# Kernel optimization log

Measured on AMD Instinct MI355X. Metric: run time of the kernel, lower is better.

The kernel has to match this reference:

```python
import jax, jax.numpy as jnp
import numpy as np

TAU = 0.5
EPS = 1e-12  # F.normalize eps


def _l2_normalize(z):
    n = jnp.linalg.norm(z, axis=1, keepdims=True)
    return z / jnp.maximum(n, EPS)


def _semi_loss(a, b):
    # a, b: [N, d], already raw embeddings; normalize then exp(sim/tau)
    an = _l2_normalize(a)
    bn = _l2_normalize(b)
    refl = jnp.exp(jnp.matmul(an, an.T) / TAU)      # [N, N]
    between = jnp.exp(jnp.matmul(an, bn.T) / TAU)   # [N, N]
    pos = jnp.diagonal(between)
    denom = refl.sum(axis=1) + between.sum(axis=1) - jnp.diagonal(refl)
    return -jnp.log(pos / denom)


def setup_inputs() -> dict:
    key = jax.random.key(0)
    k1, k2 = jax.random.split(key)
    z1 = jax.random.normal(k1, (8192, 256), dtype=jnp.float32)
    z2 = jax.random.normal(k2, (8192, 256), dtype=jnp.float32)
    return {"z1": z1, "z2": z2, "mean": 1}


def reference(z1, z2, mean):
    l1 = _semi_loss(z1, z2)
    l2 = _semi_loss(z2, z1)
    ret = (l1 + l2) * 0.5
    return ret.mean() if mean else ret.sum()
```

## Files before the change

kernel.cpp:

```cpp
#include <hip/hip_runtime.h>
#include <hip/hip_bf16.h>
#include <hip/hip_fp8.h>

#define N_ROWS 8192
#define NZ 16384
#define DIM 256
#define TAU_INV 2.0f
#define BT 128
#define NTILE 128
#define NTRI (NTILE * (NTILE + 1) / 2)
#define NCHUNK 16

typedef float f32x4 __attribute__((ext_vector_type(4)));
typedef long lx2 __attribute__((ext_vector_type(2)));

__global__ __launch_bounds__(256) void normalize_kernel(
    const float* __restrict__ z1, const float* __restrict__ z2,
    unsigned char* __restrict__ Z8, float* __restrict__ pos)
{
    const int tid = threadIdx.x;
    const int wave = tid >> 6;
    const int lane = tid & 63;
    const int row = blockIdx.x * 4 + wave;

    const float4 a = ((const float4*)(z1 + (size_t)row * DIM))[lane];
    const float4 b = ((const float4*)(z2 + (size_t)row * DIM))[lane];

    auto wsum = [&](float v) -> float {
        #pragma unroll
        for (int m = 1; m < 64; m <<= 1) v += __shfl_xor(v, m, 64);
        return v;
    };

    const float na2 = wsum(a.x*a.x + a.y*a.y + a.z*a.z + a.w*a.w);
    const float nb2 = wsum(b.x*b.x + b.y*b.y + b.z*b.z + b.w*b.w);
    const float sa = 16.0f / sqrtf(na2);
    const float sb = 16.0f / sqrtf(nb2);

    const float av[4] = {a.x*sa, a.y*sa, a.z*sa, a.w*sa};
    const float bv[4] = {b.x*sb, b.y*sb, b.z*sb, b.w*sb};
    unsigned char pa[4], pb[4];
    float qd = 0.0f;
    #pragma unroll
    for (int k = 0; k < 4; ++k) {
        __hip_fp8_e4m3 qa(av[k]);
        __hip_fp8_e4m3 qb(bv[k]);
        pa[k] = qa.__x; pb[k] = qb.__x;
        qd += float(qa) * float(qb);
    }
    const int g  = (lane >> 1) & 7;
    const int pp = ((g & 3) << 1) | (g >> 2);
    const int off = (lane >> 4) * 64 + pp * 8 + (lane & 1) * 4;
    *(uchar4*)(Z8 + (size_t)row * DIM + off) = *(uchar4*)pa;
    *(uchar4*)(Z8 + (size_t)(N_ROWS + row) * DIM + off) = *(uchar4*)pb;

    qd = wsum(qd);
    if (lane == 0) pos[row] = qd * 0.00390625f;
}

template <bool TWO_STAGE>
__global__ __launch_bounds__(256, 4) void gram_kernel(
    const unsigned char* __restrict__ Z,
    float* __restrict__ part, float* __restrict__ S)
{
    const int bid = (blockIdx.x & 7) * (NTRI / 8) + (blockIdx.x >> 3);
    int ti = (int)((257.0f - sqrtf(66049.0f - 8.0f * (float)bid)) * 0.5f);
    ti = ti < 0 ? 0 : (ti > 127 ? 127 : ti);
    while (ti * (257 - ti) / 2 > bid) --ti;
    while ((ti + 1) * (256 - ti) / 2 <= bid) ++ti;
    const int tj = ti + (bid - ti * (257 - ti) / 2);
    const bool diag = (ti == tj);

    __shared__ unsigned char Ls[32768];

    const int tid  = threadIdx.x;
    const int wave = tid >> 6;
    const int lane = tid & 63;
    const int wr = wave >> 1, wc = wave & 1;
    const int lm = lane & 15, lq = lane >> 4;

    const int r8 = lane >> 3;
    const int pg = lane & 7;
    const int G0 = pg ^ (r8 >> 1);
    const int dlt = 64 - ((G0 & 4) << 5);
    const unsigned char* pAE =
        Z + (size_t)(ti * BT + wave * 32 + r8) * DIM + (G0 << 4);
    const unsigned char* pBE =
        Z + (size_t)(tj * BT + wave * 32 + r8) * DIM + (G0 << 4);
    const unsigned char* pAO = pAE + dlt;
    const unsigned char* pBO = pBE + dlt;

    const int s0 = (lq ^ (lm >> 1)) << 4;
    const int s1 = s0 ^ 64;
    const unsigned char* LA0 = Ls + wr * 8192 + lm * 128 + s0;
    const unsigned char* LA1 = Ls + wr * 8192 + lm * 128 + s1;
    const unsigned char* LB0 = Ls + 16384 + wc * 8192 + lm * 128 + s0;
    const unsigned char* LB1 = Ls + 16384 + wc * 8192 + lm * 128 + s1;

    f32x4 acc[4][4] = {};

    #pragma unroll
    for (int kh = 0; kh < 2; ++kh) {
        if (kh) __syncthreads();
        #pragma unroll
        for (int c = 0; c < 4; ++c) {
            const int ld = (wave * 4 + c) * 1024;
            const unsigned char* ga = ((c & 1) ? pAO : pAE) + c * 2048 + kh * 128;
            const unsigned char* gb = ((c & 1) ? pBO : pBE) + c * 2048 + kh * 128;
            __builtin_amdgcn_global_load_lds(
                (const __attribute__((address_space(1))) void*)ga,
                (__attribute__((address_space(3))) void*)(Ls + ld), 16, 0, 0);
            __builtin_amdgcn_global_load_lds(
                (const __attribute__((address_space(1))) void*)gb,
                (__attribute__((address_space(3))) void*)(Ls + 16384 + ld), 16, 0, 0);
        }
        __syncthreads();

        lx2 aP[4], bP[4];
        #pragma unroll
        for (int f = 0; f < 4; ++f) {
            aP[f] = *(const lx2*)(LA0 + f * 2048);
            bP[f] = *(const lx2*)(LB0 + f * 2048);
        }
        #pragma unroll
        for (int fr = 0; fr < 4; ++fr)
            #pragma unroll
            for (int fc = 0; fc < 4; ++fc) {
                acc[fr][fc] = __builtin_amdgcn_mfma_f32_16x16x32_fp8_fp8(
                    aP[fr].x, bP[fc].x, acc[fr][fc], 0, 0, 0);
                acc[fr][fc] = __builtin_amdgcn_mfma_f32_16x16x32_fp8_fp8(
                    aP[fr].y, bP[fc].y, acc[fr][fc], 0, 0, 0);
            }
        #pragma unroll
        for (int f = 0; f < 4; ++f) {
            aP[f] = *(const lx2*)(LA1 + f * 2048);
            bP[f] = *(const lx2*)(LB1 + f * 2048);
        }
        #pragma unroll
        for (int fr = 0; fr < 4; ++fr)
            #pragma unroll
            for (int fc = 0; fc < 4; ++fc) {
                acc[fr][fc] = __builtin_amdgcn_mfma_f32_16x16x32_fp8_fp8(
                    aP[fr].x, bP[fc].x, acc[fr][fc], 0, 0, 0);
                acc[fr][fc] = __builtin_amdgcn_mfma_f32_16x16x32_fp8_fp8(
                    aP[fr].y, bP[fc].y, acc[fr][fc], 0, 0, 0);
            }
    }

    const float SC = 2.8853900817779268f / 256.0f;
    #pragma unroll
    for (int fr = 0; fr < 4; ++fr)
        #pragma unroll
        for (int fc = 0; fc < 4; ++fc)
            #pragma unroll
            for (int r = 0; r < 4; ++r)
                acc[fr][fc][r] = exp2f(acc[fr][fc][r] * SC);

    if (diag) {
        #pragma unroll
        for (int fr = 0; fr < 4; ++fr) {
            const int gi = wr * 64 + fr * 16 + lq * 4;
            #pragma unroll
            for (int fc = 0; fc < 4; ++fc) {
                const int gj = wc * 64 + fc * 16 + lm;
                #pragma unroll
                for (int r = 0; r < 4; ++r)
                    if (gj <= gi + r) acc[fr][fc][r] = 0.0f;
            }
        }
    }

    float* dst = TWO_STAGE ? (part + (size_t)bid * 512) : nullptr;

    #pragma unroll
    for (int fr = 0; fr < 4; ++fr)
        #pragma unroll
        for (int r = 0; r < 4; ++r) {
            float s = acc[fr][0][r] + acc[fr][1][r] + acc[fr][2][r] + acc[fr][3][r];
            s += __shfl_xor(s, 1, 64);
            s += __shfl_xor(s, 2, 64);
            s += __shfl_xor(s, 4, 64);
            s += __shfl_xor(s, 8, 64);
            if (lm == 0) {
                const int rr = wr * 64 + fr * 16 + lq * 4 + r;
                if (TWO_STAGE) dst[wc * 128 + rr] = s;
                else atomicAdd(&S[ti * BT + rr], s);
            }
        }
    #pragma unroll
    for (int fc = 0; fc < 4; ++fc) {
        float s = 0.0f;
        #pragma unroll
        for (int fr = 0; fr < 4; ++fr)
            #pragma unroll
            for (int r = 0; r < 4; ++r) s += acc[fr][fc][r];
        s += __shfl_xor(s, 16, 64);
        s += __shfl_xor(s, 32, 64);
        if (lq == 0) {
            const int cc = wc * 64 + fc * 16 + lm;
            if (TWO_STAGE) dst[256 + wr * 128 + cc] = s;
            else atomicAdd(&S[tj * BT + cc], s);
        }
    }
}

__global__ __launch_bounds__(256) void reduce_kernel(
    const float* __restrict__ part, float* __restrict__ S2,
    float* __restrict__ out)
{
    const int chunk = blockIdx.y;
    const int tid = threadIdx.x;
    const int r = blockIdx.x * 256 + tid;
    const int tr = r >> 7, rr = r & 127;
    const int baseRow = tr * (257 - tr) / 2;
    const int cntRow = 2 * (128 - tr);

    if (chunk == 0 && r == 0) out[0] = 0.0f;

    float s = 0.0f;
    for (int m = chunk; m < 258; m += NCHUNK) {
        size_t addr;
        if (m < cntRow) {
            const int bb = baseRow + (m >> 1);
            addr = (size_t)bb * 512 + (m & 1) * 128 + rr;
        } else {
            const int m2 = m - cntRow;
            const int tiq = m2 >> 1;
            const int bb = tiq * (257 - tiq) / 2 + (tr - tiq);
            addr = (size_t)bb * 512 + 256 + (m2 & 1) * 128 + rr;
        }
        s += part[addr];
    }
    S2[(size_t)chunk * NZ + r] = s;
}

__global__ __launch_bounds__(256) void loss2_kernel(
    const float* __restrict__ S2, const float* __restrict__ pos,
    float* __restrict__ out)
{
    const int i = blockIdx.x * 256 + threadIdx.x;
    float den1 = 0.0f, den2 = 0.0f;
    #pragma unroll
    for (int c = 0; c < NCHUNK; ++c) {
        den1 += S2[(size_t)c * NZ + i];
        den2 += S2[(size_t)c * NZ + N_ROWS + i];
    }
    float v = 0.5f * (logf(den1) + logf(den2)) - TAU_INV * pos[i];

    __shared__ float red[4];
    #pragma unroll
    for (int m = 1; m < 64; m <<= 1) v += __shfl_xor(v, m, 64);
    if ((threadIdx.x & 63) == 0) red[threadIdx.x >> 6] = v;
    __syncthreads();
    if (threadIdx.x == 0)
        atomicAdd(out, (red[0] + red[1] + red[2] + red[3]) * (1.0f / N_ROWS));
}

__global__ __launch_bounds__(256) void loss_kernel(
    const float* __restrict__ S, const float* __restrict__ pos,
    float* __restrict__ out)
{
    const int i = blockIdx.x * 256 + threadIdx.x;
    float v = 0.5f * (logf(S[i]) + logf(S[N_ROWS + i])) - TAU_INV * pos[i];

    __shared__ float red[4];
    #pragma unroll
    for (int m = 1; m < 64; m <<= 1) v += __shfl_xor(v, m, 64);
    if ((threadIdx.x & 63) == 0) red[threadIdx.x >> 6] = v;
    __syncthreads();
    if (threadIdx.x == 0)
        atomicAdd(out, (red[0] + red[1] + red[2] + red[3]) * (1.0f / N_ROWS));
}

extern "C" void kernel_launch(void* const* d_in, const int* in_sizes, int n_in,
                              void* d_out, int out_size, void* d_ws, size_t ws_size,
                              hipStream_t stream)
{
    const float* z1 = (const float*)d_in[0];
    const float* z2 = (const float*)d_in[1];
    float* out = (float*)d_out;

    char* ws = (char*)d_ws;
    unsigned char* Z8 = (unsigned char*)ws;
    float* pos  = (float*)(ws + 4194304);
    float* S2   = (float*)(ws + 4227072);
    float* part = (float*)(ws + 5275648);
    const size_t need = 5275648 + (size_t)NTRI * 512 * 4;

    normalize_kernel<<<N_ROWS / 4, 256, 0, stream>>>(z1, z2, Z8, pos);

    if (ws_size >= need) {
        gram_kernel<true><<<NTRI, 256, 0, stream>>>(Z8, part, nullptr);
        dim3 rg(NZ / 256, NCHUNK);
        reduce_kernel<<<rg, 256, 0, stream>>>(part, S2, out);
        loss2_kernel<<<N_ROWS / 256, 256, 0, stream>>>(S2, pos, out);
    } else {
        hipMemsetAsync(S2, 0, NZ * sizeof(float), stream);
        hipMemsetAsync(out, 0, sizeof(float), stream);
        gram_kernel<false><<<NTRI, 256, 0, stream>>>(Z8, nullptr, S2);
        loss_kernel<<<N_ROWS / 256, 256, 0, stream>>>(S2, pos, out);
    }
}
```

Baseline: 160.7 us.

## Process segments of four column tiles per block with resident A and double-buffered B

Each block now handles up to four consecutive upper-triangular tiles in a row, keeping the full-K A tile resident in 64KB LDS and double-buffering the B tile loads so the next tile's load overlaps current MFMA work. This cuts redundant A reloads and per-block launch/setup overhead, and adds s_setprio around MFMA sections and vectorized row-sum stores. In exchange, occupancy is halved (launch bounds 2, larger LDS) and there are fewer, longer blocks, which may hurt load balance across CUs.

Result: slower. 179.5 us (+11.7%).

```diff
diff --git a/kernel.cpp b/kernel.cpp
--- a/kernel.cpp
+++ b/kernel.cpp
@@ -10,6 +10,8 @@
 #define NTILE 128
 #define NTRI (NTILE * (NTILE + 1) / 2)
 #define NCHUNK 16
+#define SEGT 4
+#define NSEG 2112
 
 typedef float f32x4 __attribute__((ext_vector_type(4)));
 typedef long lx2 __attribute__((ext_vector_type(2)));
@@ -59,19 +61,24 @@
 }
 
 template <bool TWO_STAGE>
-__global__ __launch_bounds__(256, 4) void gram_kernel(
+__global__ __launch_bounds__(256, 2) void gram_kernel(
     const unsigned char* __restrict__ Z,
     float* __restrict__ part, float* __restrict__ S)
 {
-    const int bid = (blockIdx.x & 7) * (NTRI / 8) + (blockIdx.x >> 3);
-    int ti = (int)((257.0f - sqrtf(66049.0f - 8.0f * (float)bid)) * 0.5f);
-    ti = ti < 0 ? 0 : (ti > 127 ? 127 : ti);
-    while (ti * (257 - ti) / 2 > bid) --ti;
-    while ((ti + 1) * (256 - ti) / 2 <= bid) ++ti;
-    const int tj = ti + (bid - ti * (257 - ti) / 2);
-    const bool diag = (ti == tj);
-
-    __shared__ unsigned char Ls[32768];
+    const int sid = (blockIdx.x & 7) * (NSEG / 8) + (blockIdx.x >> 3);
+    int g = (int)((130.0f - sqrtf(16900.0f - 8.0f * (float)sid)) * 0.25f);
+    g = g < 0 ? 0 : (g > 31 ? 31 : g);
+    while (130 * g - 2 * g * g > sid) --g;
+    while (g < 31 && 130 * (g + 1) - 2 * (g + 1) * (g + 1) <= sid) ++g;
+    const int local = sid - (130 * g - 2 * g * g);
+    const int v  = 32 - g;
+    const int r4 = local / v;
+    const int s4 = local - r4 * v;
+    const int ti = 4 * g + r4;
+    const int tj0 = ti + SEGT * s4;
+    const int nt = (NTILE - tj0 < SEGT) ? (NTILE - tj0) : SEGT;
+
+    __shared__ unsigned char Ls[65536];
 
     const int tid  = threadIdx.x;
     const int wave = tid >> 6;
@@ -83,123 +90,147 @@
     const int pg = lane & 7;
     const int G0 = pg ^ (r8 >> 1);
     const int dlt = 64 - ((G0 & 4) << 5);
-    const unsigned char* pAE =
+    const unsigned char* pA =
         Z + (size_t)(ti * BT + wave * 32 + r8) * DIM + (G0 << 4);
-    const unsigned char* pBE =
-        Z + (size_t)(tj * BT + wave * 32 + r8) * DIM + (G0 << 4);
-    const unsigned char* pAO = pAE + dlt;
-    const unsigned char* pBO = pBE + dlt;
+    const unsigned char* pB0 =
+        Z + (size_t)(tj0 * BT + wave * 32 + r8) * DIM + (G0 << 4);
+
+    auto stageB = [&](const unsigned char* pb, int kh, int sl) {
+        #pragma unroll
+        for (int c = 0; c < 4; ++c) {
+            const unsigned char* gb = ((c & 1) ? pb + dlt : pb) + c * 2048 + kh * 128;
+            __builtin_amdgcn_global_load_lds(
+                (const __attribute__((address_space(1))) void*)gb,
+                (__attribute__((address_space(3))) void*)
+                    (Ls + 32768 + sl * 16384 + (wave * 4 + c) * 1024), 16, 0, 0);
+        }
+    };
+
+    #pragma unroll
+    for (int kh = 0; kh < 2; ++kh)
+        #pragma unroll
+        for (int c = 0; c < 4; ++c) {
+            const unsigned char* ga = ((c & 1) ? pA + dlt : pA) + c * 2048 + kh * 128;
+            __builtin_amdgcn_global_load_lds(
+                (const __attribute__((address_space(1))) void*)ga,
+                (__attribute__((address_space(3))) void*)
+                    (Ls + kh * 16384 + (wave * 4 + c) * 1024), 16, 0, 0);
+        }
+    stageB(pB0, 0, 0);
 
     const int s0 = (lq ^ (lm >> 1)) << 4;
     const int s1 = s0 ^ 64;
-    const unsigned char* LA0 = Ls + wr * 8192 + lm * 128 + s0;
-    const unsigned char* LA1 = Ls + wr * 8192 + lm * 128 + s1;
-    const unsigned char* LB0 = Ls + 16384 + wc * 8192 + lm * 128 + s0;
-    const unsigned char* LB1 = Ls + 16384 + wc * 8192 + lm * 128 + s1;
-
-    f32x4 acc[4][4] = {};
-
-    #pragma unroll
-    for (int kh = 0; kh < 2; ++kh) {
-        if (kh) __syncthreads();
-        #pragma unroll
-        for (int c = 0; c < 4; ++c) {
-            const int ld = (wave * 4 + c) * 1024;
-            const unsigned char* ga = ((c & 1) ? pAO : pAE) + c * 2048 + kh * 128;
-            const unsigned char* gb = ((c & 1) ? pBO : pBE) + c * 2048 + kh * 128;
-            __builtin_amdgcn_global_load_lds(
-                (const __attribute__((address_space(1))) void*)ga,
-                (__attribute__((address_space(3))) void*)(Ls + ld), 16, 0, 0);
-            __builtin_amdgcn_global_load_lds(
-                (const __attribute__((address_space(1))) void*)gb,
-                (__attribute__((address_space(3))) void*)(Ls + 16384 + ld), 16, 0, 0);
-        }
-        __syncthreads();
-
-        lx2 aP[4], bP[4];
-        #pragma unroll
-        for (int f = 0; f < 4; ++f) {
-            aP[f] = *(const lx2*)(LA0 + f * 2048);
-            bP[f] = *(const lx2*)(LB0 + f * 2048);
-        }
+    const unsigned char* LA = Ls + wr * 8192 + lm * 128;
+    const unsigned char* LB = Ls + 32768 + wc * 8192 + lm * 128;
+
+    const float SC = 2.8853900817779268f / 256.0f;
+    const int tiBase = ti * (257 - ti) / 2;
+
+    for (int t = 0; t < nt; ++t) {
+        f32x4 acc[4][4] = {};
+        #pragma unroll
+        for (int kh = 0; kh < 2; ++kh) {
+            __syncthreads();
+            if (kh == 0)            stageB(pB0 + (size_t)t * 32768, 1, 1);
+            else if (t + 1 < nt)    stageB(pB0 + (size_t)(t + 1) * 32768, 0, 0);
+
+            const unsigned char* la = LA + (kh << 14);
+            const unsigned char* lb = LB + (kh << 14);
+            lx2 aP[4], bP[4];
+            __builtin_amdgcn_s_setprio(1);
+            #pragma unroll
+            for (int f = 0; f < 4; ++f) {
+                aP[f] = *(const lx2*)(la + s0 + f * 2048);
+                bP[f] = *(const lx2*)(lb + s0 + f * 2048);
+            }
+            #pragma unroll
+            for (int fr = 0; fr < 4; ++fr)
+                #pragma unroll
+                for (int fc = 0; fc < 4; ++fc) {
+                    acc[fr][fc] = __builtin_amdgcn_mfma_f32_16x16x32_fp8_fp8(
+                        aP[fr].x, bP[fc].x, acc[fr][fc], 0, 0, 0);
+                    acc[fr][fc] = __builtin_amdgcn_mfma_f32_16x16x32_fp8_fp8(
+                        aP[fr].y, bP[fc].y, acc[fr][fc], 0, 0, 0);
+                }
+            #pragma unroll
+            for (int f = 0; f < 4; ++f) {
+                aP[f] = *(const lx2*)(la + s1 + f * 2048);
+                bP[f] = *(const lx2*)(lb + s1 + f * 2048);
+            }
+            #pragma unroll
+            for (int fr = 0; fr < 4; ++fr)
+                #pragma unroll
+                for (int fc = 0; fc < 4; ++fc) {
+                    acc[fr][fc] = __builtin_amdgcn_mfma_f32_16x16x32_fp8_fp8(
+                        aP[fr].x, bP[fc].x, acc[fr][fc], 0, 0, 0);
+                    acc[fr][fc] = __builtin_amdgcn_mfma_f32_16x16x32_fp8_fp8(
+                        aP[fr].y, bP[fc].y, acc[fr][fc], 0, 0, 0);
+                }
+            __builtin_amdgcn_s_setprio(0);
+        }
+
         #pragma unroll
         for (int fr = 0; fr < 4; ++fr)
             #pragma unroll
-            for (int fc = 0; fc < 4; ++fc) {
-                acc[fr][fc] = __builtin_amdgcn_mfma_f32_16x16x32_fp8_fp8(
-                    aP[fr].x, bP[fc].x, acc[fr][fc], 0, 0, 0);
-                acc[fr][fc] = __builtin_amdgcn_mfma_f32_16x16x32_fp8_fp8(
-                    aP[fr].y, bP[fc].y, acc[fr][fc], 0, 0, 0);
-            }
-        #pragma unroll
-        for (int f = 0; f < 4; ++f) {
-            aP[f] = *(const lx2*)(LA1 + f * 2048);
-            bP[f] = *(const lx2*)(LB1 + f * 2048);
-        }
-        #pragma unroll
-        for (int fr = 0; fr < 4; ++fr)
-            #pragma unroll
-            for (int fc = 0; fc < 4; ++fc) {
-                acc[fr][fc] = __builtin_amdgcn_mfma_f32_16x16x32_fp8_fp8(
-                    aP[fr].x, bP[fc].x, acc[fr][fc], 0, 0, 0);
-                acc[fr][fc] = __builtin_amdgcn_mfma_f32_16x16x32_fp8_fp8(
-                    aP[fr].y, bP[fc].y, acc[fr][fc], 0, 0, 0);
-            }
-    }
-
-    const float SC = 2.8853900817779268f / 256.0f;
-    #pragma unroll
-    for (int fr = 0; fr < 4; ++fr)
-        #pragma unroll
-        for (int fc = 0; fc < 4; ++fc)
-            #pragma unroll
-            for (int r = 0; r < 4; ++r)
-                acc[fr][fc][r] = exp2f(acc[fr][fc][r] * SC);
-
-    if (diag) {
+            for (int fc = 0; fc < 4; ++fc)
+                #pragma unroll
+                for (int r = 0; r < 4; ++r)
+                    acc[fr][fc][r] = exp2f(acc[fr][fc][r] * SC);
+
+        const int tj = tj0 + t;
+        if (ti == tj) {
+            #pragma unroll
+            for (int fr = 0; fr < 4; ++fr) {
+                const int gi = wr * 64 + fr * 16 + lq * 4;
+                #pragma unroll
+                for (int fc = 0; fc < 4; ++fc) {
+                    const int gj = wc * 64 + fc * 16 + lm;
+                    #pragma unroll
+                    for (int r = 0; r < 4; ++r)
+                        if (gj <= gi + r) acc[fr][fc][r] = 0.0f;
+                }
+            }
+        }
+
+        float* dst = TWO_STAGE ? (part + (size_t)(tiBase + (tj - ti)) * 512)
+                               : nullptr;
+
         #pragma unroll
         for (int fr = 0; fr < 4; ++fr) {
-            const int gi = wr * 64 + fr * 16 + lq * 4;
-            #pragma unroll
-            for (int fc = 0; fc < 4; ++fc) {
-                const int gj = wc * 64 + fc * 16 + lm;
-                #pragma unroll
-                for (int r = 0; r < 4; ++r)
-                    if (gj <= gi + r) acc[fr][fc][r] = 0.0f;
-            }
-        }
-    }
-
-    float* dst = TWO_STAGE ? (part + (size_t)bid * 512) : nullptr;
-
-    #pragma unroll
-    for (int fr = 0; fr < 4; ++fr)
-        #pragma unroll
-        for (int r = 0; r < 4; ++r) {
-            float s = acc[fr][0][r] + acc[fr][1][r] + acc[fr][2][r] + acc[fr][3][r];
-            s += __shfl_xor(s, 1, 64);
-            s += __shfl_xor(s, 2, 64);
-            s += __shfl_xor(s, 4, 64);
-            s += __shfl_xor(s, 8, 64);
+            f32x4 rs;
+            #pragma unroll
+            for (int r = 0; r < 4; ++r) {
+                float s = acc[fr][0][r] + acc[fr][1][r] + acc[fr][2][r] + acc[fr][3][r];
+                s += __shfl_xor(s, 1, 64);
+                s += __shfl_xor(s, 2, 64);
+                s += __shfl_xor(s, 4, 64);
+                s += __shfl_xor(s, 8, 64);
+                rs[r] = s;
+            }
             if (lm == 0) {
-                const int rr = wr * 64 + fr * 16 + lq * 4 + r;
-                if (TWO_STAGE) dst[wc * 128 + rr] = s;
-                else atomicAdd(&S[ti * BT + rr], s);
-            }
-        }
-    #pragma unroll
-    for (int fc = 0; fc < 4; ++fc) {
-        float s = 0.0f;
-        #pragma unroll
-        for (int fr = 0; fr < 4; ++fr)
-            #pragma unroll
-            for (int r = 0; r < 4; ++r) s += acc[fr][fc][r];
-        s += __shfl_xor(s, 16, 64);
-        s += __shfl_xor(s, 32, 64);
-        if (lq == 0) {
-            const int cc = wc * 64 + fc * 16 + lm;
-            if (TWO_STAGE) dst[256 + wr * 128 + cc] = s;
-            else atomicAdd(&S[tj * BT + cc], s);
+                const int rr = wr * 64 + fr * 16 + lq * 4;
+                if (TWO_STAGE) *(f32x4*)(dst + wc * 128 + rr) = rs;
+                else {
+                    #pragma unroll
+                    for (int r = 0; r < 4; ++r)
+                        atomicAdd(&S[ti * BT + rr + r], rs[r]);
+                }
+            }
+        }
+        #pragma unroll
+        for (int fc = 0; fc < 4; ++fc) {
+            float s = 0.0f;
+            #pragma unroll
+            for (int fr = 0; fr < 4; ++fr)
+                #pragma unroll
+                for (int r = 0; r < 4; ++r) s += acc[fr][fc][r];
+            s += __shfl_xor(s, 16, 64);
+            s += __shfl_xor(s, 32, 64);
+            if (lq == 0) {
+                const int cc = wc * 64 + fc * 16 + lm;
+                if (TWO_STAGE) dst[256 + wr * 128 + cc] = s;
+                else atomicAdd(&S[tj * BT + cc], s);
+            }
         }
     }
 }
@@ -290,14 +321,14 @@
     normalize_kernel<<<N_ROWS / 4, 256, 0, stream>>>(z1, z2, Z8, pos);
 
     if (ws_size >= need) {
-        gram_kernel<true><<<NTRI, 256, 0, stream>>>(Z8, part, nullptr);
+        gram_kernel<true><<<NSEG, 256, 0, stream>>>(Z8, part, nullptr);
         dim3 rg(NZ / 256, NCHUNK);
         reduce_kernel<<<rg, 256, 0, stream>>>(part, S2, out);
         loss2_kernel<<<N_ROWS / 256, 256, 0, stream>>>(S2, pos, out);
     } else {
         hipMemsetAsync(S2, 0, NZ * sizeof(float), stream);
         hipMemsetAsync(out, 0, sizeof(float), stream);
-        gram_kernel<false><<<NTRI, 256, 0, stream>>>(Z8, nullptr, S2);
+        gram_kernel<false><<<NSEG, 256, 0, stream>>>(Z8, nullptr, S2);
         loss_kernel<<<N_ROWS / 256, 256, 0, stream>>>(S2, pos, out);
     }
 }
```
